# Kernel optimization log

Measured on AMD Instinct MI355X. Metric: run time of the kernel, lower is better.

Reference implementation:

```python
import jax, jax.numpy as jnp
import numpy as np

B, K, PS, DP = 8, 8, 128, 16           # batch, patches/example, patch px, dino patch size
D, NH, HD, L = 1024, 8, 128, 2         # embed dim, heads, head dim, transformer layers
GRID = PS // DP                        # 8 tokens per side
TPP = GRID * GRID                      # 64 tokens per patch


def _conv(x, w, stride, pad):
    return jax.lax.conv_general_dilated(x, w, (stride, stride), pad,
                                        dimension_numbers=('NCHW', 'OIHW', 'NCHW'))


def _ln(x, g, b, eps=1e-5):
    m = jnp.mean(x, -1, keepdims=True)
    v = jnp.var(x, -1, keepdims=True)
    return (x - m) * jax.lax.rsqrt(v + eps) * g + b


def _bn(x, g, b, m, v, eps=1e-5):
    inv = jax.lax.rsqrt(v + eps)
    return (x - m[:, None, None]) * inv[:, None, None] * g[:, None, None] + b[:, None, None]


def _up2(x):  # bilinear x2, align_corners=False (half-pixel, matches jax.image.resize)
    n, c, h, w = x.shape
    return jax.image.resize(x, (n, c, 2 * h, 2 * w), method='linear')


def _mha(x, wqkv, bqkv, wo, bo):
    b, s, d = x.shape
    qkv = x @ wqkv.T + bqkv
    q, k, v = jnp.split(qkv, 3, axis=-1)
    q = q.reshape(b, s, NH, HD).transpose(0, 2, 1, 3)
    k = k.reshape(b, s, NH, HD).transpose(0, 2, 1, 3)
    v = v.reshape(b, s, NH, HD).transpose(0, 2, 1, 3)
    att = jax.nn.softmax(jnp.einsum('bhqd,bhkd->bhqk', q, k) / jnp.sqrt(jnp.float32(HD)), axis=-1)
    o = jnp.einsum('bhqk,bhkd->bhqd', att, v).transpose(0, 2, 1, 3).reshape(b, s, d)
    return o @ wo.T + bo


def setup_inputs() -> dict:
    key = jax.random.key(0)
    ks = iter(jax.random.split(key, 40))

    def rn(shape, s=0.02):
        return jax.random.normal(next(ks), shape, jnp.float32) * s

    inp = {}
    inp['patches'] = jax.random.normal(next(ks), (B, K, 3, PS, PS), jnp.float32)
    inp['pe_w'] = rn((D, 3, DP, DP))
    inp['pe_b'] = jnp.zeros((D,), jnp.float32)
    inp['qkv_w'] = rn((L, 3 * D, D))
    inp['qkv_b'] = jnp.zeros((L, 3 * D), jnp.float32)
    inp['out_w'] = rn((L, D, D))
    inp['out_b'] = jnp.zeros((L, D), jnp.float32)
    inp['ln1_g'] = jnp.ones((L, D), jnp.float32)
    inp['ln1_b'] = jnp.zeros((L, D), jnp.float32)
    inp['ff1_w'] = rn((L, 4 * D, D))
    inp['ff1_b'] = jnp.zeros((L, 4 * D), jnp.float32)
    inp['ff2_w'] = rn((L, D, 4 * D))
    inp['ff2_b'] = jnp.zeros((L, D), jnp.float32)
    inp['ln2_g'] = jnp.ones((L, D), jnp.float32)
    inp['ln2_b'] = jnp.zeros((L, D), jnp.float32)
    chans = [(512, D), (256, 512), (128, 256), (64, 128)]
    for i, (co, ci) in enumerate(chans, 1):
        inp[f'dw{i}'] = rn((co, ci, 3, 3), 0.05)
        inp[f'db{i}'] = jnp.zeros((co,), jnp.float32)
        inp[f'g{i}'] = jnp.ones((co,), jnp.float32)
        inp[f'be{i}'] = jnp.zeros((co,), jnp.float32)
        inp[f'm{i}'] = jnp.zeros((co,), jnp.float32)
        inp[f'v{i}'] = jnp.ones((co,), jnp.float32)
    inp['dw5'] = rn((1, 64, 1, 1), 0.05)
    inp['db5'] = jnp.zeros((1,), jnp.float32)
    return inp


def reference(patches, pe_w, pe_b, qkv_w, qkv_b, out_w, out_b, ln1_g, ln1_b,
              ff1_w, ff1_b, ff2_w, ff2_b, ln2_g, ln2_b,
              dw1, db1, g1, be1, m1, v1, dw2, db2, g2, be2, m2, v2,
              dw3, db3, g3, be3, m3, v3, dw4, db4, g4, be4, m4, v4, dw5, db5):
    b, k = patches.shape[:2]
    x = patches.reshape(b * k, 3, PS, PS)
    # frozen DINO patch embedding (runs under torch.no_grad in the original)
    hs = _conv(x, pe_w, DP, 'VALID') + pe_b[None, :, None, None]     # [BK, D, GRID, GRID]
    hs = jax.lax.stop_gradient(hs)
    hs = hs.reshape(b * k, D, TPP).transpose(0, 2, 1).reshape(b, k * TPP, D)
    # post-norm TransformerEncoder (norm_first=False, gelu), dropout=eval (identity)
    for i in range(L):
        hs = _ln(hs + _mha(hs, qkv_w[i], qkv_b[i], out_w[i], out_b[i]), ln1_g[i], ln1_b[i])
        ff = jax.nn.gelu(hs @ ff1_w[i].T + ff1_b[i], approximate=False) @ ff2_w[i].T + ff2_b[i]
        hs = _ln(hs + ff, ln2_g[i], ln2_b[i])
    fm = hs.reshape(b * k, TPP, D).transpose(0, 2, 1).reshape(b * k, D, GRID, GRID)
    # CNN decoder: (conv3x3 -> BN(eval) -> ReLU -> bilinear x2) x4 -> conv1x1
    y = _up2(jax.nn.relu(_bn(_conv(fm, dw1, 1, 'SAME') + db1[None, :, None, None], g1, be1, m1, v1)))
    y = _up2(jax.nn.relu(_bn(_conv(y, dw2, 1, 'SAME') + db2[None, :, None, None], g2, be2, m2, v2)))
    y = _up2(jax.nn.relu(_bn(_conv(y, dw3, 1, 'SAME') + db3[None, :, None, None], g3, be3, m3, v3)))
    y = _up2(jax.nn.relu(_bn(_conv(y, dw4, 1, 'SAME') + db4[None, :, None, None], g4, be4, m4, v4)))
    y = _conv(y, dw5, 1, 'VALID') + db5[None, :, None, None]          # [BK, 1, PS, PS]
    return y.reshape(b, k, 1, PS, PS)
```

## Files before the change

### kernel.cpp

```cpp
#include <hip/hip_runtime.h>
#include <stdint.h>


typedef unsigned short u16;
typedef __bf16 bf16x8 __attribute__((ext_vector_type(8)));
typedef short  s16x8  __attribute__((ext_vector_type(8)));
typedef float  f32x4  __attribute__((ext_vector_type(4)));

__device__ __forceinline__ float b2f(u16 x) { return __uint_as_float(((unsigned)x) << 16); }
__device__ __forceinline__ u16 f2b(float f) {
  unsigned u = __float_as_uint(f);
  unsigned r = (u + 0x7fffu + ((u >> 16) & 1u)) >> 16;
  return (u16)r;
}
__device__ __forceinline__ void async16(u16* lds, const u16* g) {
  __builtin_amdgcn_global_load_lds((const __attribute__((address_space(1))) void*)g,
                                   (__attribute__((address_space(3))) void*)lds, 16, 0, 0);
}
__device__ __forceinline__ float gelu_f(float x) {
  return 0.5f * x * (1.0f + erff(x * 0.70710678118654752f));
}

__global__ __launch_bounds__(256) void cvt_f2b(const float* __restrict__ src,
                                               u16* __restrict__ dst, int n) {
  const int i = (blockIdx.x * 256 + threadIdx.x) * 4;
  if (i + 3 < n) {
    const float4 v = *(const float4*)(src + i);
    dst[i] = f2b(v.x); dst[i + 1] = f2b(v.y); dst[i + 2] = f2b(v.z); dst[i + 3] = f2b(v.w);
  }
}

__global__ __launch_bounds__(256) void gemm_bt(
    const u16* __restrict__ A, int lda, long long sAb, long long sAh,
    const u16* __restrict__ B, int ldb, long long sBb, long long sBh,
    u16* __restrict__ Cb, int ldc, long long sCb, long long sCh,
    const float* __restrict__ bias, int epi, int ZH, int nk)
{
  __shared__ u16 As[128 * 32];
  __shared__ u16 Bs[128 * 32];
  const int tid = threadIdx.x;
  const int zb = blockIdx.z / ZH, zh = blockIdx.z % ZH;
  const u16* Ab = A + zb * sAb + zh * sAh;
  const u16* Bb = B + zb * sBb + zh * sBh;
  const int m0 = blockIdx.y << 7, n0 = blockIdx.x << 7;
  const int wave = tid >> 6, lane = tid & 63;
  const int wm = (wave >> 1) << 6, wn = (wave & 1) << 6;
  const int lr = lane & 15, lq = lane >> 4;
  const int rowb = tid >> 2, kc = (tid & 3) << 3;

  f32x4 acc[4][4] = {};

  for (int kt = 0; kt < nk; ++kt) {
    const int k0 = kt << 5;
    __syncthreads();
    async16(&As[tid * 8],         Ab + (long long)(m0 + rowb)      * lda + (k0 + kc));
    async16(&As[(tid + 256) * 8], Ab + (long long)(m0 + rowb + 64) * lda + (k0 + kc));
    async16(&Bs[tid * 8],         Bb + (long long)(n0 + rowb)      * ldb + (k0 + kc));
    async16(&Bs[(tid + 256) * 8], Bb + (long long)(n0 + rowb + 64) * ldb + (k0 + kc));
    __syncthreads();

    bf16x8 af[4], bfv[4];
#pragma unroll
    for (int mi = 0; mi < 4; ++mi)
      af[mi] = __builtin_bit_cast(bf16x8, *(const s16x8*)&As[((wm + mi * 16 + lr) << 5) + (lq << 3)]);
#pragma unroll
    for (int ni = 0; ni < 4; ++ni)
      bfv[ni] = __builtin_bit_cast(bf16x8, *(const s16x8*)&Bs[((wn + ni * 16 + lr) << 5) + (lq << 3)]);
#pragma unroll
    for (int mi = 0; mi < 4; ++mi)
#pragma unroll
      for (int ni = 0; ni < 4; ++ni)
        acc[mi][ni] = __builtin_amdgcn_mfma_f32_16x16x32_bf16(af[mi], bfv[ni], acc[mi][ni], 0, 0, 0);
  }

  const long long Co = zb * sCb + zh * sCh;
#pragma unroll
  for (int ni = 0; ni < 4; ++ni) {
    const int col = n0 + wn + ni * 16 + lr;
    const float badd = bias ? bias[col] : 0.0f;
#pragma unroll
    for (int mi = 0; mi < 4; ++mi) {
      const int row0 = m0 + wm + mi * 16 + (lq << 2);
#pragma unroll
      for (int r = 0; r < 4; ++r) {
        float v = acc[mi][ni][r] + badd;
        if (epi == 1) v = gelu_f(v);
        Cb[Co + (long long)(row0 + r) * ldc + col] = f2b(v);
      }
    }
  }
}

__global__ __launch_bounds__(256) void conv_gemm(
    const u16* __restrict__ U, const u16* __restrict__ Wr,
    u16* __restrict__ Out,
    const float* __restrict__ bn_g, const float* __restrict__ bn_b,
    const float* __restrict__ bn_m, const float* __restrict__ bn_v,
    const float* __restrict__ cb,
    const u16* __restrict__ zpg,
    int H, int W, int l2w, int l2hw, int l2c, int CoutReal, int Kdim, int nk)
{
  __shared__ u16 As[3][128 * 32];
  __shared__ u16 Bs[3][64 * 32];
  const int tid = threadIdx.x;
  const int m0 = blockIdx.y << 7, n0 = blockIdx.x << 6;
  const int wave = tid >> 6, lane = tid & 63;
  const int wm = (wave >> 1) << 6, wn = (wave & 1) << 5;
  const int lr = lane & 15, lq = lane >> 4;
  const int rowb = tid >> 2;
  const int kc_e = (((tid & 3) ^ ((tid >> 3) & 3)) << 3);
  const int kslot = ((lq ^ ((lr >> 1) & 3)) << 3);
  const int hwmask = (1 << l2hw) - 1, wmask = (1 << l2w) - 1, cmask = (1 << l2c) - 1;

  int yA[2], xA[2];
  long long baseA[2];
  {
#pragma unroll
    for (int i = 0; i < 2; ++i) {
      const int mrow = m0 + rowb + (i << 6);
      const int img = mrow >> l2hw;
      const int rem = mrow & hwmask;
      yA[i] = rem >> l2w; xA[i] = rem & wmask;
      baseA[i] = (long long)(img << l2hw);
    }
  }
  const u16* Bbase = Wr + (long long)(n0 + rowb) * Kdim + kc_e;

  f32x4 acc[4][2] = {};

  auto stage = [&](int kt, int b) {
    const int k0 = kt << 5;
    const int k = k0 + kc_e;
    const int t = k >> l2c, ci = k & cmask;
    const int dy = (t * 86) >> 8;
    const int dx = t - dy * 3;
#pragma unroll
    for (int i = 0; i < 2; ++i) {
      const int yy = yA[i] + dy - 1, xx = xA[i] + dx - 1;
      const u16* src = ((unsigned)yy < (unsigned)H && (unsigned)xx < (unsigned)W)
          ? U + (((baseA[i] + (yy << l2w) + xx) << l2c) + ci)
          : zpg;
      async16(&As[b][(tid + (i << 8)) * 8], src);
    }
    async16(&Bs[b][tid * 8], Bbase + k0);
  };

  stage(0, 0);
  stage(1, 1);

  for (int t0 = 0; t0 < nk; t0 += 3) {
#pragma unroll
    for (int p = 0; p < 3; ++p) {
      const int tt = t0 + p;
      if (tt + 2 < nk) {
        stage(tt + 2, (p + 2) % 3);
        asm volatile("s_waitcnt vmcnt(6)" ::: "memory");
      } else if (tt + 1 < nk) {
        asm volatile("s_waitcnt vmcnt(3)" ::: "memory");
      } else {
        asm volatile("s_waitcnt vmcnt(0)" ::: "memory");
      }
      asm volatile("s_barrier" ::: "memory");

      bf16x8 af[4], bfv[2];
#pragma unroll
      for (int mi = 0; mi < 4; ++mi)
        af[mi] = __builtin_bit_cast(bf16x8, *(const s16x8*)&As[p][((wm + mi * 16 + lr) << 5) + kslot]);
#pragma unroll
      for (int ni = 0; ni < 2; ++ni)
        bfv[ni] = __builtin_bit_cast(bf16x8, *(const s16x8*)&Bs[p][((wn + ni * 16 + lr) << 5) + kslot]);
#pragma unroll
      for (int mi = 0; mi < 4; ++mi)
#pragma unroll
        for (int ni = 0; ni < 2; ++ni)
          acc[mi][ni] = __builtin_amdgcn_mfma_f32_16x16x32_bf16(af[mi], bfv[ni], acc[mi][ni], 0, 0, 0);

      asm volatile("s_barrier" ::: "memory");
    }
  }

#pragma unroll
  for (int ni = 0; ni < 2; ++ni) {
    const int col = n0 + wn + ni * 16 + lr;
    const bool ok = col < CoutReal;
    float bs = 0.0f, bsh = 0.0f;
    if (ok) {
      const float inv = rsqrtf(bn_v[col] + 1e-5f);
      bs = bn_g[col] * inv;
      bsh = (cb[col] - bn_m[col]) * bs + bn_b[col];
    }
#pragma unroll
    for (int mi = 0; mi < 4; ++mi) {
      const int row0 = m0 + wm + mi * 16 + (lq << 2);
#pragma unroll
      for (int r = 0; r < 4; ++r) {
        if (ok) {
          const float v = fmaxf(acc[mi][ni][r] * bs + bsh, 0.0f);
          Out[(long long)(row0 + r) * CoutReal + col] = f2b(v);
        }
      }
    }
  }
}


__global__ void pe_gather(const float* __restrict__ patches, u16* __restrict__ Ape) {
  const int t = blockIdx.x, tid = threadIdx.x;
  const int img = t >> 6, pos = t & 63, ty = pos >> 3, tx = pos & 7;
  const float* base = patches + (long long)img * 3 * 128 * 128;
  u16* dst = Ape + (long long)t * 768;
  for (int k = tid; k < 768; k += 256) {
    const int c = k >> 8, rr = k & 255, ky = rr >> 4, kx = rr & 15;
    dst[k] = f2b(base[c * 16384 + (ty * 16 + ky) * 128 + tx * 16 + kx]);
  }
}

__global__ void vt_transpose(const u16* __restrict__ qkv, u16* __restrict__ Vt) {
  __shared__ u16 lds[64 * 130];
  const int tt = blockIdx.x;
  const int z = blockIdx.y;
  const int bq = z >> 3, h = z & 7;
  const int tid = threadIdx.x;
  for (int idx = tid; idx < 64 * 128; idx += 256) {
    const int t = idx >> 7, d = idx & 127;
    lds[t * 130 + d] = qkv[(long long)(bq * 512 + tt * 64 + t) * 3072 + 2048 + h * 128 + d];
  }
  __syncthreads();
  for (int idx = tid; idx < 64 * 128; idx += 256) {
    const int d = idx >> 6, t = idx & 63;
    Vt[(long long)z * 65536 + d * 512 + tt * 64 + t] = lds[t * 130 + d];
  }
}

__global__ __launch_bounds__(256) void softmax_rows(u16* __restrict__ P) {
  __shared__ float red[8];
  const long long base = (long long)blockIdx.x * 512;
  const int tid = threadIdx.x;
  const float sc = 0.08838834764831845f;
  float x0 = b2f(P[base + tid]) * sc;
  float x1 = b2f(P[base + tid + 256]) * sc;
  float mx = fmaxf(x0, x1);
  for (int o = 32; o; o >>= 1) mx = fmaxf(mx, __shfl_down(mx, o));
  if ((tid & 63) == 0) red[tid >> 6] = mx;
  __syncthreads();
  mx = fmaxf(fmaxf(red[0], red[1]), fmaxf(red[2], red[3]));
  const float e0 = expf(x0 - mx), e1 = expf(x1 - mx);
  float s = e0 + e1;
  for (int o = 32; o; o >>= 1) s += __shfl_down(s, o);
  __syncthreads();
  if ((tid & 63) == 0) red[tid >> 6] = s;
  __syncthreads();
  s = red[0] + red[1] + red[2] + red[3];
  const float inv = 1.0f / s;
  P[base + tid] = f2b(e0 * inv);
  P[base + tid + 256] = f2b(e1 * inv);
}

__global__ __launch_bounds__(256) void ln_kernel(
    u16* __restrict__ hsb, const u16* __restrict__ P,
    const float* __restrict__ gw, const float* __restrict__ bw)
{
  __shared__ float red[8];
  const int r = blockIdx.x, tid = threadIdx.x;
  float x[4], s = 0.0f, s2 = 0.0f;
#pragma unroll
  for (int i = 0; i < 4; ++i) {
    const int c = tid + i * 256;
    const float v = b2f(hsb[(long long)r * 1024 + c]) + b2f(P[(long long)r * 1024 + c]);
    x[i] = v; s += v; s2 += v * v;
  }
  for (int o = 32; o; o >>= 1) { s += __shfl_down(s, o); s2 += __shfl_down(s2, o); }
  if ((tid & 63) == 0) { red[tid >> 6] = s; red[4 + (tid >> 6)] = s2; }
  __syncthreads();
  s  = red[0] + red[1] + red[2] + red[3];
  s2 = red[4] + red[5] + red[6] + red[7];
  const float mean = s * (1.0f / 1024.0f);
  const float var = s2 * (1.0f / 1024.0f) - mean * mean;
  const float inv = rsqrtf(var + 1e-5f);
#pragma unroll
  for (int i = 0; i < 4; ++i) {
    const int c = tid + i * 256;
    const float y = (x[i] - mean) * inv * gw[c] + bw[c];
    hsb[(long long)r * 1024 + c] = f2b(y);
  }
}

__global__ void repack_w(const float* __restrict__ src, u16* __restrict__ dst, int Cout, int l2c) {
  const int co = blockIdx.x, tid = threadIdx.x;
  const int Cin = 1 << l2c, K9 = 9 << l2c;
  for (int j = tid; j < K9; j += 256) {
    const int t = j >> l2c, ci = j & (Cin - 1);
    u16 v = 0;
    if (co < Cout) v = f2b(src[(long long)(co * Cin + ci) * 9 + t]);
    dst[(long long)co * K9 + j] = v;
  }
}

__global__ void ups2x(const u16* __restrict__ in, u16* __restrict__ out,
                      int l2h, int l2w, int l2c, long long total)
{
  const long long idx = (long long)blockIdx.x * 256 + threadIdx.x;
  if (idx >= total) return;
  const int H = 1 << l2h, W = 1 << l2w, C = 1 << l2c;
  const int c = (int)(idx & (C - 1));
  long long t = idx >> l2c;
  const int ox = (int)(t & (2 * W - 1)); t >>= (l2w + 1);
  const int oy = (int)(t & (2 * H - 1)); t >>= (l2h + 1);
  const int img = (int)t;
  const int iy = oy >> 1, ix = ox >> 1;
  int y0, y1, x0, x1; float wy0, wy1, wx0, wx1;
  if (oy & 1) { y0 = iy; y1 = min(iy + 1, H - 1); wy0 = 0.75f; wy1 = 0.25f; }
  else        { y0 = max(iy - 1, 0); y1 = iy;     wy0 = 0.25f; wy1 = 0.75f; }
  if (ox & 1) { x0 = ix; x1 = min(ix + 1, W - 1); wx0 = 0.75f; wx1 = 0.25f; }
  else        { x0 = max(ix - 1, 0); x1 = ix;     wx0 = 0.25f; wx1 = 0.75f; }
  const u16* base = in + (((long long)img) << (l2h + l2w + l2c));
  const float v00 = b2f(base[((((long long)y0 << l2w) + x0) << l2c) + c]);
  const float v01 = b2f(base[((((long long)y0 << l2w) + x1) << l2c) + c]);
  const float v10 = b2f(base[((((long long)y1 << l2w) + x0) << l2c) + c]);
  const float v11 = b2f(base[((((long long)y1 << l2w) + x1) << l2c) + c]);
  out[idx] = f2b(wy0 * (wx0 * v00 + wx1 * v01) + wy1 * (wx0 * v10 + wx1 * v11));
}

__global__ __launch_bounds__(256) void conv1x1_final(
    const u16* __restrict__ C4, const float* __restrict__ w5,
    const float* __restrict__ b5, float* __restrict__ Z)
{
  const int tid = threadIdx.x;
  const int px = blockIdx.x * 4 + (tid >> 6);
  const int lane = tid & 63;
  float v = b2f(C4[(long long)px * 64 + lane]) * w5[lane];
  for (int o = 32; o; o >>= 1) v += __shfl_down(v, o);
  if (lane == 0) Z[px] = v + b5[0];
}

__global__ void ups_final(const float* __restrict__ Z, float* __restrict__ out) {
  const int idx = blockIdx.x * 256 + threadIdx.x;
  const int ox = idx & 127, oy = (idx >> 7) & 127, img = idx >> 14;
  const int iy = oy >> 1, ix = ox >> 1;
  int y0, y1, x0, x1; float wy0, wy1, wx0, wx1;
  if (oy & 1) { y0 = iy; y1 = min(iy + 1, 63); wy0 = 0.75f; wy1 = 0.25f; }
  else        { y0 = max(iy - 1, 0); y1 = iy;  wy0 = 0.25f; wy1 = 0.75f; }
  if (ox & 1) { x0 = ix; x1 = min(ix + 1, 63); wx0 = 0.75f; wx1 = 0.25f; }
  else        { x0 = max(ix - 1, 0); x1 = ix;  wx0 = 0.25f; wx1 = 0.75f; }
  const float* zi = Z + (long long)img * 4096;
  const float v = wy0 * (wx0 * zi[y0 * 64 + x0] + wx1 * zi[y0 * 64 + x1]) +
                  wy1 * (wx0 * zi[y1 * 64 + x0] + wx1 * zi[y1 * 64 + x1]);
  out[idx] = v;
}

extern "C" void kernel_launch(void* const* d_in, const int* in_sizes, int n_in,
                              void* d_out, int out_size, void* d_ws, size_t ws_size,
                              hipStream_t stream)
{
  (void)in_sizes; (void)n_in; (void)out_size;
  if (ws_size < 110395648u) return;
  const float* patches = (const float*)d_in[0];
  const float* pe_w = (const float*)d_in[1];
  const float* pe_b = (const float*)d_in[2];
  const float* qkv_w = (const float*)d_in[3];
  const float* qkv_b = (const float*)d_in[4];
  const float* out_w = (const float*)d_in[5];
  const float* out_b = (const float*)d_in[6];
  const float* ln1_g = (const float*)d_in[7];
  const float* ln1_b = (const float*)d_in[8];
  const float* ff1_w = (const float*)d_in[9];
  const float* ff1_b = (const float*)d_in[10];
  const float* ff2_w = (const float*)d_in[11];
  const float* ff2_b = (const float*)d_in[12];
  const float* ln2_g = (const float*)d_in[13];
  const float* ln2_b = (const float*)d_in[14];
  const float* dwv[4] = {(const float*)d_in[15], (const float*)d_in[21], (const float*)d_in[27], (const float*)d_in[33]};
  const float* dbv[4] = {(const float*)d_in[16], (const float*)d_in[22], (const float*)d_in[28], (const float*)d_in[34]};
  const float* gv[4]  = {(const float*)d_in[17], (const float*)d_in[23], (const float*)d_in[29], (const float*)d_in[35]};
  const float* bev[4] = {(const float*)d_in[18], (const float*)d_in[24], (const float*)d_in[30], (const float*)d_in[36]};
  const float* mv[4]  = {(const float*)d_in[19], (const float*)d_in[25], (const float*)d_in[31], (const float*)d_in[37]};
  const float* vv[4]  = {(const float*)d_in[20], (const float*)d_in[26], (const float*)d_in[32], (const float*)d_in[38]};
  const float* dw5 = (const float*)d_in[39];
  const float* db5 = (const float*)d_in[40];
  float* outp = (float*)d_out;
  char* ws = (char*)d_ws;

  u16* HS_B = (u16*)(ws + 0);
  u16* APE  = (u16*)(ws + 8388608);
  u16* QKV  = (u16*)(ws + 8388608);
  u16* VT   = (u16*)(ws + 33554432);
  u16* SF   = (u16*)(ws + 41943040);
  u16* FF1G = (u16*)(ws + 41943040);
  u16* ATT  = (u16*)(ws + 75497472);
  u16* P_B  = (u16*)(ws + 83886080);
  u16* W1   = (u16*)(ws + 92274688);
  u16* W2   = (u16*)(ws + 100663296);
  u16* WR1 = (u16*)(ws + 8388608);
  u16* WR2 = (u16*)(ws + 17825792);
  u16* WR3 = (u16*)(ws + 20185088);
  u16* C1  = (u16*)(ws + 20774912);
  u16* U1  = (u16*)(ws + 24969216);
  u16* C2  = (u16*)(ws + 41746432);
  u16* U2  = (u16*)(ws + 50135040);
  u16* C3  = (u16*)(ws + 83689472);
  u16* U3  = (u16*)(ws + 8388608);
  u16* C4  = (u16*)(ws + 75497472);
  u16* ZPG = (u16*)(ws + 109051904);
  u16* WR4 = (u16*)(ws + 109052160);
  float* Z = (float*)(ws + 109347072);

  pe_gather<<<4096, 256, 0, stream>>>(patches, APE);
  cvt_f2b<<<768, 256, 0, stream>>>(pe_w, W1, 786432);
  gemm_bt<<<dim3(8, 32, 1), 256, 0, stream>>>(
      APE, 768, 0, 0, W1, 768, 0, 0,
      HS_B, 1024, 0, 0, pe_b, 0, 1, 24);

  for (int l = 0; l < 2; ++l) {
    cvt_f2b<<<3072, 256, 0, stream>>>(qkv_w + (long long)l * 3145728, W1, 3145728);
    gemm_bt<<<dim3(24, 32, 1), 256, 0, stream>>>(
        HS_B, 1024, 0, 0, W1, 1024, 0, 0,
        QKV, 3072, 0, 0, qkv_b + l * 3072, 0, 1, 32);
    vt_transpose<<<dim3(8, 64), 256, 0, stream>>>(QKV, VT);
    gemm_bt<<<dim3(4, 4, 64), 256, 0, stream>>>(
        QKV, 3072, 1572864, 128, QKV + 1024, 3072, 1572864, 128,
        SF, 512, 2097152, 262144, nullptr, 0, 8, 4);
    softmax_rows<<<32768, 256, 0, stream>>>(SF);
    gemm_bt<<<dim3(1, 4, 64), 256, 0, stream>>>(
        SF, 512, 2097152, 262144, VT, 512, 524288, 65536,
        ATT, 1024, 524288, 128, nullptr, 0, 8, 16);
    cvt_f2b<<<1024, 256, 0, stream>>>(out_w + (long long)l * 1048576, W2, 1048576);
    gemm_bt<<<dim3(8, 32, 1), 256, 0, stream>>>(
        ATT, 1024, 0, 0, W2, 1024, 0, 0,
        P_B, 1024, 0, 0, out_b + l * 1024, 0, 1, 32);
    ln_kernel<<<4096, 256, 0, stream>>>(HS_B, P_B, ln1_g + l * 1024, ln1_b + l * 1024);
    cvt_f2b<<<4096, 256, 0, stream>>>(ff1_w + (long long)l * 4194304, W1, 4194304);
    cvt_f2b<<<4096, 256, 0, stream>>>(ff2_w + (long long)l * 4194304, W2, 4194304);
    gemm_bt<<<dim3(32, 32, 1), 256, 0, stream>>>(
        HS_B, 1024, 0, 0, W1, 1024, 0, 0,
        FF1G, 4096, 0, 0, ff1_b + l * 4096, 1, 1, 32);
    gemm_bt<<<dim3(8, 32, 1), 256, 0, stream>>>(
        FF1G, 4096, 0, 0, W2, 4096, 0, 0,
        P_B, 1024, 0, 0, ff2_b + l * 1024, 0, 1, 128);
    ln_kernel<<<4096, 256, 0, stream>>>(HS_B, P_B, ln2_g + l * 1024, ln2_b + l * 1024);
  }

  hipMemsetAsync((void*)ZPG, 0, 256, stream);
  repack_w<<<512, 256, 0, stream>>>(dwv[0], WR1, 512, 10);
  repack_w<<<256, 256, 0, stream>>>(dwv[1], WR2, 256, 9);
  repack_w<<<128, 256, 0, stream>>>(dwv[2], WR3, 128, 8);
  repack_w<<<128, 256, 0, stream>>>(dwv[3], WR4, 64, 7);

  conv_gemm<<<dim3(8, 32, 1), 256, 0, stream>>>(
      HS_B, WR1, C1, gv[0], bev[0], mv[0], vv[0], dbv[0], ZPG,
      8, 8, 3, 6, 10, 512, 9216, 288);
  ups2x<<<32768, 256, 0, stream>>>(C1, U1, 3, 3, 9, 8388608LL);
  conv_gemm<<<dim3(4, 128, 1), 256, 0, stream>>>(
      U1, WR2, C2, gv[1], bev[1], mv[1], vv[1], dbv[1], ZPG,
      16, 16, 4, 8, 9, 256, 4608, 144);
  ups2x<<<65536, 256, 0, stream>>>(C2, U2, 4, 4, 8, 16777216LL);
  conv_gemm<<<dim3(2, 512, 1), 256, 0, stream>>>(
      U2, WR3, C3, gv[2], bev[2], mv[2], vv[2], dbv[2], ZPG,
      32, 32, 5, 10, 8, 128, 2304, 72);
  ups2x<<<131072, 256, 0, stream>>>(C3, U3, 5, 5, 7, 33554432LL);
  conv_gemm<<<dim3(1, 2048, 1), 256, 0, stream>>>(
      U3, WR4, C4, gv[3], bev[3], mv[3], vv[3], dbv[3], ZPG,
      64, 64, 6, 12, 7, 64, 1152, 36);
  conv1x1_final<<<65536, 256, 0, stream>>>(C4, dw5, db5, Z);
  ups_final<<<4096, 256, 0, stream>>>(Z, outp);
}
```

Baseline: 1.458 ms.

## Triple-buffer gemm_bt with async LDS prefetch and swizzle; swap conv_gemm grid axes

The generic bf16 GEMM gains a 3-stage LDS ring filled by async global-to-LDS loads two k-tiles ahead. Explicit vmcnt waits and raw barriers replace the two full syncthreads per iteration, so global latency overlaps the MFMA work. An XOR swizzle on the k-slot is meant to reduce LDS bank conflicts. The conv GEMM grid is also transposed so M tiles walk the fastest block index, which changes how weight and activation tiles are reused across concurrently running blocks. The cost is three times the LDS footprint in gemm_bt, which may lower occupancy.

```diff
diff --git a/kernel.cpp b/kernel.cpp
--- a/kernel.cpp
+++ b/kernel.cpp
@@ -36,8 +36,8 @@
     u16* __restrict__ Cb, int ldc, long long sCb, long long sCh,
     const float* __restrict__ bias, int epi, int ZH, int nk)
 {
-  __shared__ u16 As[128 * 32];
-  __shared__ u16 Bs[128 * 32];
+  __shared__ u16 As[3][128 * 32];
+  __shared__ u16 Bs[3][128 * 32];
   const int tid = threadIdx.x;
   const int zb = blockIdx.z / ZH, zh = blockIdx.z % ZH;
   const u16* Ab = A + zb * sAb + zh * sAh;
@@ -46,31 +46,55 @@
   const int wave = tid >> 6, lane = tid & 63;
   const int wm = (wave >> 1) << 6, wn = (wave & 1) << 6;
   const int lr = lane & 15, lq = lane >> 4;
-  const int rowb = tid >> 2, kc = (tid & 3) << 3;
+  const int rowb = tid >> 2;
+  const int kc_e = (((tid & 3) ^ ((tid >> 3) & 3)) << 3);
+  const int kslot = ((lq ^ ((lr >> 1) & 3)) << 3);
+
+  const u16* Arow0 = Ab + (long long)(m0 + rowb)      * lda + kc_e;
+  const u16* Arow1 = Ab + (long long)(m0 + rowb + 64) * lda + kc_e;
+  const u16* Brow0 = Bb + (long long)(n0 + rowb)      * ldb + kc_e;
+  const u16* Brow1 = Bb + (long long)(n0 + rowb + 64) * ldb + kc_e;
 
   f32x4 acc[4][4] = {};
 
+  auto stage = [&](int kt, int b) {
+    const int k0 = kt << 5;
+    async16(&As[b][tid * 8],         Arow0 + k0);
+    async16(&As[b][(tid + 256) * 8], Arow1 + k0);
+    async16(&Bs[b][tid * 8],         Brow0 + k0);
+    async16(&Bs[b][(tid + 256) * 8], Brow1 + k0);
+  };
+
+  stage(0, 0);
+  if (nk > 1) stage(1, 1);
+  int cur = 0;
   for (int kt = 0; kt < nk; ++kt) {
-    const int k0 = kt << 5;
-    __syncthreads();
-    async16(&As[tid * 8],         Ab + (long long)(m0 + rowb)      * lda + (k0 + kc));
-    async16(&As[(tid + 256) * 8], Ab + (long long)(m0 + rowb + 64) * lda + (k0 + kc));
-    async16(&Bs[tid * 8],         Bb + (long long)(n0 + rowb)      * ldb + (k0 + kc));
-    async16(&Bs[(tid + 256) * 8], Bb + (long long)(n0 + rowb + 64) * ldb + (k0 + kc));
-    __syncthreads();
+    if (kt + 2 < nk) {
+      int nb = cur + 2; if (nb >= 3) nb -= 3;
+      stage(kt + 2, nb);
+      asm volatile("s_waitcnt vmcnt(8)" ::: "memory");
+    } else if (kt + 1 < nk) {
+      asm volatile("s_waitcnt vmcnt(4)" ::: "memory");
+    } else {
+      asm volatile("s_waitcnt vmcnt(0)" ::: "memory");
+    }
+    asm volatile("s_barrier" ::: "memory");
 
     bf16x8 af[4], bfv[4];
 #pragma unroll
     for (int mi = 0; mi < 4; ++mi)
-      af[mi] = __builtin_bit_cast(bf16x8, *(const s16x8*)&As[((wm + mi * 16 + lr) << 5) + (lq << 3)]);
+      af[mi] = __builtin_bit_cast(bf16x8, *(const s16x8*)&As[cur][((wm + mi * 16 + lr) << 5) + kslot]);
 #pragma unroll
     for (int ni = 0; ni < 4; ++ni)
-      bfv[ni] = __builtin_bit_cast(bf16x8, *(const s16x8*)&Bs[((wn + ni * 16 + lr) << 5) + (lq << 3)]);
+      bfv[ni] = __builtin_bit_cast(bf16x8, *(const s16x8*)&Bs[cur][((wn + ni * 16 + lr) << 5) + kslot]);
 #pragma unroll
     for (int mi = 0; mi < 4; ++mi)
 #pragma unroll
       for (int ni = 0; ni < 4; ++ni)
         acc[mi][ni] = __builtin_amdgcn_mfma_f32_16x16x32_bf16(af[mi], bfv[ni], acc[mi][ni], 0, 0, 0);
+
+    asm volatile("s_barrier" ::: "memory");
+    ++cur; if (cur == 3) cur = 0;
   }
 
   const long long Co = zb * sCb + zh * sCh;
@@ -103,7 +127,7 @@
   __shared__ u16 As[3][128 * 32];
   __shared__ u16 Bs[3][64 * 32];
   const int tid = threadIdx.x;
-  const int m0 = blockIdx.y << 7, n0 = blockIdx.x << 6;
+  const int m0 = blockIdx.x << 7, n0 = blockIdx.y << 6;
   const int wave = tid >> 6, lane = tid & 63;
   const int wm = (wave >> 1) << 6, wn = (wave & 1) << 5;
   const int lr = lane & 15, lq = lane >> 4;
@@ -445,19 +469,19 @@
   repack_w<<<128, 256, 0, stream>>>(dwv[2], WR3, 128, 8);
   repack_w<<<128, 256, 0, stream>>>(dwv[3], WR4, 64, 7);
 
-  conv_gemm<<<dim3(8, 32, 1), 256, 0, stream>>>(
+  conv_gemm<<<dim3(32, 8, 1), 256, 0, stream>>>(
       HS_B, WR1, C1, gv[0], bev[0], mv[0], vv[0], dbv[0], ZPG,
       8, 8, 3, 6, 10, 512, 9216, 288);
   ups2x<<<32768, 256, 0, stream>>>(C1, U1, 3, 3, 9, 8388608LL);
-  conv_gemm<<<dim3(4, 128, 1), 256, 0, stream>>>(
+  conv_gemm<<<dim3(128, 4, 1), 256, 0, stream>>>(
       U1, WR2, C2, gv[1], bev[1], mv[1], vv[1], dbv[1], ZPG,
       16, 16, 4, 8, 9, 256, 4608, 144);
   ups2x<<<65536, 256, 0, stream>>>(C2, U2, 4, 4, 8, 16777216LL);
-  conv_gemm<<<dim3(2, 512, 1), 256, 0, stream>>>(
+  conv_gemm<<<dim3(512, 2, 1), 256, 0, stream>>>(
       U2, WR3, C3, gv[2], bev[2], mv[2], vv[2], dbv[2], ZPG,
       32, 32, 5, 10, 8, 128, 2304, 72);
   ups2x<<<131072, 256, 0, stream>>>(C3, U3, 5, 5, 7, 33554432LL);
-  conv_gemm<<<dim3(1, 2048, 1), 256, 0, stream>>>(
+  conv_gemm<<<dim3(2048, 1, 1), 256, 0, stream>>>(
       U3, WR4, C4, gv[3], bev[3], mv[3], vv[3], dbv[3], ZPG,
       64, 64, 6, 12, 7, 64, 1152, 36);
   conv1x1_final<<<65536, 256, 0, stream>>>(C4, dw5, db5, Z);
```

New measurement: 1.396 ms. 4.2% less time.
